# Optimization experiments

Hardware: AMD Instinct MI355X
Metric: run time of the kernel (lower is better)

The kernel has to match this reference:

```python
import jax, jax.numpy as jnp
import numpy as np

L, E, H, FF, N, S, ML = 6, 768, 12, 3072, 8, 1023, 2048


def setup_inputs() -> dict:
    key = jax.random.key(0)
    ks = jax.random.split(key, 16)
    rn = lambda k, shape, s=0.02: jax.random.normal(k, shape, jnp.float32) * s
    return {
        "x": jax.random.normal(ks[0], (N, S, E), jnp.float32),
        "mask": jnp.ones((N, 1, 1, S + 1), jnp.int32),
        "pos_emb": rn(ks[1], (ML, E), 1.0),
        "cls": rn(ks[2], (1, 1, E), 1.0),
        "Wq": rn(ks[3], (L, E, E)), "bq": jnp.zeros((L, E), jnp.float32),
        "Wk": rn(ks[4], (L, E, E)), "bk": jnp.zeros((L, E), jnp.float32),
        "Wv": rn(ks[5], (L, E, E)), "bv": jnp.zeros((L, E), jnp.float32),
        "Wo": rn(ks[6], (L, E, E)), "bo": jnp.zeros((L, E), jnp.float32),
        "ln1_g": jnp.ones((L, E), jnp.float32), "ln1_b": jnp.zeros((L, E), jnp.float32),
        "ln2_g": jnp.ones((L, E), jnp.float32), "ln2_b": jnp.zeros((L, E), jnp.float32),
        "Wf1": rn(ks[7], (L, E, FF)), "bf1": jnp.zeros((L, FF), jnp.float32),
        "Wf2": rn(ks[8], (L, FF, E)), "bf2": jnp.zeros((L, E), jnp.float32),
    }


def _ln(x, g, b, eps=1e-5):
    m = x.mean(-1, keepdims=True)
    v = ((x - m) ** 2).mean(-1, keepdims=True)
    return (x - m) / jnp.sqrt(v + eps) * g + b


def reference(x, mask, pos_emb, cls, Wq, bq, Wk, bk, Wv, bv, Wo, bo,
              ln1_g, ln1_b, ln2_g, ln2_b, Wf1, bf1, Wf2, bf2):
    n, s, e = x.shape
    h = H
    d = e // h
    # prepend CLS token -> [N, T, E], add learned positions
    x = jnp.concatenate([jnp.broadcast_to(cls, (n, 1, e)), x], axis=1)
    t = s + 1
    out = x + pos_emb[:t][None]
    scale = jnp.float32(1.0 / np.sqrt(d))
    for i in range(Wq.shape[0]):
        q = (out @ Wq[i] + bq[i]).reshape(n, t, h, d)
        k = (out @ Wk[i] + bk[i]).reshape(n, t, h, d)
        v = (out @ Wv[i] + bv[i]).reshape(n, t, h, d)
        energy = jnp.einsum('nqhd,nkhd->nhqk', q, k)  # [N,H,T,T]
        energy = jnp.where(mask == 0, jnp.float32(-1e20), energy)
        attn = jax.nn.softmax(energy * scale, axis=-1)
        att = jnp.einsum('nhqk,nkhd->nqhd', attn, v).reshape(n, t, e)
        att = att @ Wo[i] + bo[i]
        hid = _ln(att + out, ln1_g[i], ln1_b[i])  # residual uses query (=out)
        ff = jax.nn.gelu(hid @ Wf1[i] + bf1[i], approximate=False) @ Wf2[i] + bf2[i]
        out = _ln(ff + hid, ln2_g[i], ln2_b[i])
    return out
```

## Files before the change

kernel.cpp:

```cpp
#include <hip/hip_runtime.h>

#define L_ 6
#define E_ 768
#define H_ 12
#define FF_ 3072

typedef __attribute__((ext_vector_type(8))) short bh8;
typedef __attribute__((ext_vector_type(4))) float f32x4;

__device__ inline ushort f2bf(float f) {
  unsigned u = __builtin_bit_cast(unsigned, f);
  u += 0x7fffu + ((u >> 16) & 1u);
  return (ushort)(u >> 16);
}

__device__ __forceinline__ void gload16(const void* g, void* l) {
  __builtin_amdgcn_global_load_lds(
      (const __attribute__((address_space(1))) void*)g,
      (__attribute__((address_space(3))) void*)l, 16, 0, 0);
}

__global__ __launch_bounds__(256) void pack_bias(const float* __restrict__ bq,
                                                 const float* __restrict__ bk,
                                                 const float* __restrict__ bv,
                                                 float* __restrict__ bqkv) {
  int idx = blockIdx.x * 256 + threadIdx.x;
  int l = idx / 2304, j = idx % 2304;
  float v = (j < 768) ? bq[l * 768 + j]
          : (j < 1536) ? bk[l * 768 + j - 768]
                       : bv[l * 768 + j - 1536];
  bqkv[idx] = v;
}

__global__ __launch_bounds__(256) void transpose_w(const float* __restrict__ src,
                                                   ushort* __restrict__ dst,
                                                   int K, int Nn,
                                                   long sstride, long dstride) {
  src += (long)blockIdx.z * sstride;
  dst += (long)blockIdx.z * dstride;
  __shared__ float t[32][33];
  int tx = threadIdx.x & 31, ty = threadIdx.x >> 5;
  int kb = blockIdx.x * 32, nb = blockIdx.y * 32;
#pragma unroll
  for (int i = 0; i < 4; i++) {
    int kr = ty + i * 8;
    t[kr][tx] = src[(long)(kb + kr) * Nn + nb + tx];
  }
  __syncthreads();
#pragma unroll
  for (int i = 0; i < 4; i++) {
    int nr = ty + i * 8;
    dst[(long)(nb + nr) * K + kb + tx] = f2bf(t[tx][nr]);
  }
}

__global__ __launch_bounds__(256) void embed_k(const float* __restrict__ x,
                                               const float* __restrict__ pos,
                                               const float* __restrict__ cls,
                                               float* __restrict__ res,
                                               ushort* __restrict__ xb) {
  int idx = blockIdx.x * 256 + threadIdx.x;
  int c4 = idx % 192;
  int row = idx / 192;
  int t = row & 1023, n = row >> 10;
  f32x4 pv = ((const f32x4*)pos)[t * 192 + c4];
  f32x4 xv;
  if (t == 0) xv = ((const f32x4*)cls)[c4];
  else        xv = ((const f32x4*)x)[(size_t)(n * 1023 + t - 1) * 192 + c4];
  f32x4 s = xv + pv;
  ((f32x4*)res)[idx] = s;
  ushort4 h;
  h.x = f2bf(s[0]); h.y = f2bf(s[1]); h.z = f2bf(s[2]); h.w = f2bf(s[3]);
  ((ushort4*)xb)[idx] = h;
}

template <int MODE>
__global__ __launch_bounds__(256, 4) void gemm_bt(const ushort* __restrict__ A,
                                                  const ushort* __restrict__ Bt,
                                                  int M, int N, int K,
                                                  const float* __restrict__ bias,
                                                  float* __restrict__ sp0,
                                                  float* __restrict__ sp1,
                                                  float* __restrict__ sp2,
                                                  float* __restrict__ sp3,
                                                  ushort* __restrict__ out16,
                                                  ushort* __restrict__ vtb,
                                                  int ksl) {
  __shared__ ushort As[128 * 64];
  __shared__ ushort Bs[128 * 64];
  int tid = threadIdx.x;
  int wid = tid >> 6, lane = tid & 63;
  int wm = wid >> 1, wn = wid & 1;
  int l15 = lane & 15, lhi = lane >> 4;
  int ln8 = lane >> 3, lc8 = (lane & 7) * 8;
  int row0 = blockIdx.x * 128, col0 = blockIdx.y * 128;
  int kb = (MODE == 3) ? blockIdx.z * ksl : 0;
  int nt = ((MODE == 3) ? ksl : K) >> 6;

  f32x4 acc[4][4];
#pragma unroll
  for (int i = 0; i < 4; i++)
#pragma unroll
    for (int j = 0; j < 4; j++) acc[i][j] = (f32x4){0.f, 0.f, 0.f, 0.f};

  const ushort* Ap = A + (size_t)(row0 + wid * 32 + ln8) * K + kb + lc8;
  const ushort* Bp = Bt + (size_t)(col0 + wid * 32 + ln8) * K + kb + lc8;

  for (int kt = 0; kt < nt; ++kt) {
    int k0 = kt << 6;
#pragma unroll
    for (int p = 0; p < 4; p++) {
      int r = wid * 32 + p * 8;
      gload16(Ap + (size_t)p * 8 * K + k0, As + r * 64);
      gload16(Bp + (size_t)p * 8 * K + k0, Bs + r * 64);
    }
    __syncthreads();
#pragma unroll
    for (int ks = 0; ks < 2; ks++) {
      bh8 af[4], bfr[4];
#pragma unroll
      for (int i = 0; i < 4; i++)
        af[i] = *(const bh8*)(As + (wm * 64 + i * 16 + l15) * 64 + ks * 32 + lhi * 8);
#pragma unroll
      for (int j = 0; j < 4; j++)
        bfr[j] = *(const bh8*)(Bs + (wn * 64 + j * 16 + l15) * 64 + ks * 32 + lhi * 8);
#pragma unroll
      for (int i = 0; i < 4; i++)
#pragma unroll
        for (int j = 0; j < 4; j++)
          acc[i][j] = __builtin_amdgcn_mfma_f32_16x16x32_bf16(af[i], bfr[j], acc[i][j], 0, 0, 0);
    }
    __syncthreads();
  }

  float* outp = nullptr;
  if (MODE == 3)
    outp = (blockIdx.z == 0) ? sp0 : (blockIdx.z == 1) ? sp1 : (blockIdx.z == 2) ? sp2 : sp3;
#pragma unroll
  for (int j = 0; j < 4; j++) {
    int col = col0 + wn * 64 + j * 16 + l15;
    float bv = (MODE == 3) ? 0.f : bias[col];
#pragma unroll
    for (int i = 0; i < 4; i++) {
      int rbase = row0 + wm * 64 + i * 16 + lhi * 4;
      if (MODE == 0 && col >= 1536) {
        int hd = col - 1536;
        int nn = rbase >> 10, t0 = rbase & 1023;
        ushort4 h4;
        h4.x = f2bf(acc[i][j][0] + bv);
        h4.y = f2bf(acc[i][j][1] + bv);
        h4.z = f2bf(acc[i][j][2] + bv);
        h4.w = f2bf(acc[i][j][3] + bv);
        *(ushort4*)(vtb + ((size_t)nn * 768 + hd) * 1024 + t0) = h4;
      } else {
#pragma unroll
        for (int r = 0; r < 4; r++) {
          int row = rbase + r;
          size_t o = (size_t)row * N + col;
          float v = acc[i][j][r] + bv;
          if (MODE == 0) {
            out16[o] = f2bf(v);
          } else if (MODE == 3) {
            outp[o] = v;
          } else {
            v = 0.5f * v * (1.f + erff(v * 0.70710678118f));
            out16[o] = f2bf(v);
          }
        }
      }
    }
  }
}

__global__ __launch_bounds__(256) void attn_k(const ushort* __restrict__ qkv,
                                              const ushort* __restrict__ vtb,
                                              const int* __restrict__ mask,
                                              ushort* __restrict__ attb) {
  int qt = blockIdx.x, h = blockIdx.y, n = blockIdx.z;
  int tid = threadIdx.x, wid = tid >> 6, lane = tid & 63;
  int l15 = lane & 15, lhi = lane >> 4;
  __shared__ ushort Ks[2][64 * 64];
  __shared__ ushort Vs[2][64 * 64];
  __shared__ ushort Pt[4][16 * 64];
  ushort* Pw = Pt[wid];

  int ln8 = lane >> 3;
  int swc = (((lane & 7) ^ ln8) << 3);

  const ushort* Kg = qkv + 768 + h * 64;
  const ushort* Vg = vtb + (size_t)(n * 768 + h * 64) * 1024;

  auto stage = [&](int b, int kv0) {
#pragma unroll
    for (int it = 0; it < 2; ++it) {
      int r = wid * 16 + it * 8;
      gload16(Kg + (size_t)(n * 1024 + kv0 + r + ln8) * 2304 + swc, &Ks[b][r * 64]);
      gload16(Vg + (size_t)(r + ln8) * 1024 + kv0 + swc, &Vs[b][r * 64]);
    }
  };

  stage(0, 0);

  int q0 = qt * 64 + wid * 16;
  size_t rowQ = (size_t)(n * 1024 + q0 + l15) * 2304 + h * 64;
  bh8 qf0 = *(const bh8*)(qkv + rowQ + lhi * 8);
  bh8 qf1 = *(const bh8*)(qkv + rowQ + 32 + lhi * 8);

  unsigned long long mbits = 0ull;
#pragma unroll
  for (int i = 0; i < 64; ++i)
    mbits |= (unsigned long long)(mask[n * 1024 + i * 16 + l15] != 0) << i;

  bh8 ones;
#pragma unroll
  for (int i = 0; i < 8; ++i) ones[i] = (short)0x3F80;

  f32x4 o[4], lacc = (f32x4){0.f, 0.f, 0.f, 0.f};
#pragma unroll
  for (int i = 0; i < 4; i++) o[i] = (f32x4){0.f, 0.f, 0.f, 0.f};

  int x15 = (l15 & 7) << 3;
  int buf = 0;
  for (int t = 0; t < 16; ++t) {
    if (t < 15) {
      stage(buf ^ 1, (t + 1) * 64);
      asm volatile("s_waitcnt vmcnt(4)" ::: "memory");
    } else {
      asm volatile("s_waitcnt vmcnt(0)" ::: "memory");
    }
    __builtin_amdgcn_s_barrier();
    const ushort* Kb = Ks[buf];
    const ushort* Vb = Vs[buf];

    f32x4 s[4];
    __builtin_amdgcn_s_setprio(1);
#pragma unroll
    for (int t4 = 0; t4 < 4; ++t4) {
      int rs = (t4 * 16 + l15) * 64;
      s[t4] = (f32x4){0.f, 0.f, 0.f, 0.f};
      s[t4] = __builtin_amdgcn_mfma_f32_16x16x32_bf16(qf0, *(const bh8*)(Kb + rs + ((lhi << 3) ^ x15)), s[t4], 0, 0, 0);
      s[t4] = __builtin_amdgcn_mfma_f32_16x16x32_bf16(qf1, *(const bh8*)(Kb + rs + (((4 + lhi) << 3) ^ x15)), s[t4], 0, 0, 0);
    }
    __builtin_amdgcn_s_setprio(0);

#pragma unroll
    for (int t4 = 0; t4 < 4; ++t4) {
      bool mk = (mbits >> (t * 4 + t4)) & 1ull;
#pragma unroll
      for (int r = 0; r < 4; r++) {
        float xv = mk ? s[t4][r] * 0.125f : -1e20f;
        float p = __expf(fminf(xv, 80.f));
        int prow = lhi * 4 + r;
        int slot = t4 * 2 + (l15 >> 3);
        Pw[prow * 64 + (((slot ^ (prow & 7)) << 3) | (l15 & 7))] = f2bf(p);
      }
    }

    bh8 pf0 = *(const bh8*)(Pw + l15 * 64 + ((lhi << 3) ^ x15));
    bh8 pf1 = *(const bh8*)(Pw + l15 * 64 + (((4 + lhi) << 3) ^ x15));
    __builtin_amdgcn_s_setprio(1);
#pragma unroll
    for (int nb = 0; nb < 4; nb++) {
      int rs = (nb * 16 + l15) * 64;
      o[nb] = __builtin_amdgcn_mfma_f32_16x16x32_bf16(pf0, *(const bh8*)(Vb + rs + ((lhi << 3) ^ x15)), o[nb], 0, 0, 0);
      o[nb] = __builtin_amdgcn_mfma_f32_16x16x32_bf16(pf1, *(const bh8*)(Vb + rs + (((4 + lhi) << 3) ^ x15)), o[nb], 0, 0, 0);
    }
    lacc = __builtin_amdgcn_mfma_f32_16x16x32_bf16(pf0, ones, lacc, 0, 0, 0);
    lacc = __builtin_amdgcn_mfma_f32_16x16x32_bf16(pf1, ones, lacc, 0, 0, 0);
    __builtin_amdgcn_s_setprio(0);

    if (t < 15) {
      asm volatile("s_waitcnt lgkmcnt(0)" ::: "memory");
      __builtin_amdgcn_s_barrier();
    }
    buf ^= 1;
  }

#pragma unroll
  for (int nb = 0; nb < 4; nb++)
#pragma unroll
    for (int r = 0; r < 4; r++) {
      float val = o[nb][r] / lacc[r];
      int row = q0 + lhi * 4 + r;
      int col = h * 64 + nb * 16 + l15;
      attb[(size_t)(n * 1024 + row) * 768 + col] = f2bf(val);
    }
}

template <int S>
__global__ __launch_bounds__(256) void ln_red_k(const float* __restrict__ p0,
                                                const float* __restrict__ p1,
                                                const float* __restrict__ p2,
                                                const float* __restrict__ p3,
                                                const float* __restrict__ resid,
                                                const float* __restrict__ bias,
                                                const float* __restrict__ g,
                                                const float* __restrict__ b,
                                                float* __restrict__ y32,
                                                ushort* __restrict__ y16) {
  int row = blockIdx.x, tid = threadIdx.x;
  size_t base = (size_t)row * 768;
  float v[3];
#pragma unroll
  for (int i = 0; i < 3; i++) {
    int c = tid + i * 256;
    float s = resid[base + c] + bias[c];
    s += p0[base + c] + p1[base + c];
    if (S > 2) s += p2[base + c];
    if (S > 3) s += p3[base + c];
    v[i] = s;
  }
  float s = v[0] + v[1] + v[2];
  float sq = v[0] * v[0] + v[1] * v[1] + v[2] * v[2];
#pragma unroll
  for (int off = 32; off > 0; off >>= 1) {
    s += __shfl_down(s, off);
    sq += __shfl_down(sq, off);
  }
  __shared__ float sws[4], swq[4];
  int wid = tid >> 6, lane = tid & 63;
  if (lane == 0) { sws[wid] = s; swq[wid] = sq; }
  __syncthreads();
  float ts = sws[0] + sws[1] + sws[2] + sws[3];
  float tq = swq[0] + swq[1] + swq[2] + swq[3];
  float mean = ts * (1.f / 768.f);
  float var = tq * (1.f / 768.f) - mean * mean;
  float rstd = rsqrtf(var + 1e-5f);
#pragma unroll
  for (int i = 0; i < 3; i++) {
    int c = tid + i * 256;
    float y = (v[i] - mean) * rstd * g[c] + b[c];
    y32[base + c] = y;
    y16[base + c] = f2bf(y);
  }
}

extern "C" void kernel_launch(void* const* d_in, const int* in_sizes, int n_in,
                              void* d_out, int out_size, void* d_ws, size_t ws_size,
                              hipStream_t stream) {
  const float* x    = (const float*)d_in[0];
  const int*   mask = (const int*)d_in[1];
  const float* pos  = (const float*)d_in[2];
  const float* cls  = (const float*)d_in[3];
  const float* Wq   = (const float*)d_in[4];
  const float* bq   = (const float*)d_in[5];
  const float* Wk   = (const float*)d_in[6];
  const float* bk   = (const float*)d_in[7];
  const float* Wv   = (const float*)d_in[8];
  const float* bv   = (const float*)d_in[9];
  const float* Wo   = (const float*)d_in[10];
  const float* bo   = (const float*)d_in[11];
  const float* ln1g = (const float*)d_in[12];
  const float* ln1b = (const float*)d_in[13];
  const float* ln2g = (const float*)d_in[14];
  const float* ln2b = (const float*)d_in[15];
  const float* Wf1  = (const float*)d_in[16];
  const float* bf1  = (const float*)d_in[17];
  const float* Wf2  = (const float*)d_in[18];
  const float* bf2  = (const float*)d_in[19];

  char* ws = (char*)d_ws;
  size_t off = 0;
  auto alloc = [&](size_t bytes) {
    char* p = ws + off;
    off += (bytes + 255) & ~(size_t)255;
    return p;
  };
  const size_t M = 8192;
  ushort* qkvt = (ushort*)alloc((size_t)L_ * 2304 * 768 * 2);
  ushort* wot  = (ushort*)alloc((size_t)L_ * 768 * 768 * 2);
  ushort* wf1t = (ushort*)alloc((size_t)L_ * 3072 * 768 * 2);
  ushort* wf2t = (ushort*)alloc((size_t)L_ * 768 * 3072 * 2);
  float*  bqkv = (float*)alloc((size_t)L_ * 2304 * 4);
  float*  res  = (float*)alloc(M * 768 * 4);
  float*  pre  = (float*)alloc(M * 768 * 4);
  ushort* xb   = (ushort*)alloc(M * 768 * 2);
  ushort* qkvb = (ushort*)alloc(M * 2304 * 2);
  ushort* vtb  = (ushort*)alloc(M * 768 * 2);
  ushort* attb = (ushort*)alloc(M * 768 * 2);
  ushort* ffb  = (ushort*)alloc(M * 3072 * 2);
  (void)ws_size; (void)in_sizes; (void)n_in; (void)out_size;

  float* slA = pre;
  float* slB = (float*)qkvb;
  float* slC = (float*)((char*)qkvb + M * 768 * 4);
  float* slD = (float*)ffb;

  dim3 tb(256);
  pack_bias<<<54, tb, 0, stream>>>(bq, bk, bv, bqkv);
  transpose_w<<<dim3(24, 24, 6), tb, 0, stream>>>(Wq, qkvt,              768, 768, 768L * 768, 2304L * 768);
  transpose_w<<<dim3(24, 24, 6), tb, 0, stream>>>(Wk, qkvt + 768 * 768,  768, 768, 768L * 768, 2304L * 768);
  transpose_w<<<dim3(24, 24, 6), tb, 0, stream>>>(Wv, qkvt + 2 * 768 * 768, 768, 768, 768L * 768, 2304L * 768);
  transpose_w<<<dim3(24, 24, 6), tb, 0, stream>>>(Wo, wot, 768, 768, 768L * 768, 768L * 768);
  transpose_w<<<dim3(24, 96, 6), tb, 0, stream>>>(Wf1, wf1t, 768, 3072, 768L * 3072, 3072L * 768);
  transpose_w<<<dim3(96, 24, 6), tb, 0, stream>>>(Wf2, wf2t, 3072, 768, 3072L * 768, 768L * 3072);
  embed_k<<<6144, tb, 0, stream>>>(x, pos, cls, res, xb);

  for (int l = 0; l < L_; l++) {
    gemm_bt<0><<<dim3(64, 18), tb, 0, stream>>>(xb, qkvt + (size_t)l * 2304 * 768,
                                                8192, 2304, 768, bqkv + l * 2304,
                                                nullptr, nullptr, nullptr, nullptr,
                                                qkvb, vtb, 0);
    attn_k<<<dim3(16, 12, 8), tb, 0, stream>>>(qkvb, vtb, mask, attb);
    gemm_bt<3><<<dim3(64, 6, 4), tb, 0, stream>>>(attb, wot + (size_t)l * 768 * 768,
                                                  8192, 768, 768, nullptr,
                                                  slA, slB, slC, slD,
                                                  nullptr, nullptr, 192);
    ln_red_k<4><<<8192, tb, 0, stream>>>(slA, slB, slC, slD, res, bo + l * 768,
                                         ln1g + l * 768, ln1b + l * 768, res, xb);
    gemm_bt<2><<<dim3(64, 24), tb, 0, stream>>>(xb, wf1t + (size_t)l * 3072 * 768,
                                                8192, 3072, 768, bf1 + l * 3072,
                                                nullptr, nullptr, nullptr, nullptr,
                                                ffb, nullptr, 0);
    float* y32 = (l == L_ - 1) ? (float*)d_out : res;
    gemm_bt<3><<<dim3(64, 6, 3), tb, 0, stream>>>(ffb, wf2t + (size_t)l * 768 * 3072,
                                                  8192, 768, 3072, nullptr,
                                                  slA, slB, slC, nullptr,
                                                  nullptr, nullptr, 1024);
    ln_red_k<3><<<8192, tb, 0, stream>>>(slA, slB, slC, nullptr, res, bf2 + l * 768,
                                         ln2g + l * 768, ln2b + l * 768, y32, xb);
  }
}
```

Baseline: 2.042 ms.

## Add 256x256 double-buffered swizzled GEMM for QKV, FF1 and FF2 projections

```diff
diff --git a/kernel.cpp b/kernel.cpp
--- a/kernel.cpp
+++ b/kernel.cpp
@@ -75,74 +75,117 @@
 }
 
 template <int MODE>
-__global__ __launch_bounds__(256, 4) void gemm_bt(const ushort* __restrict__ A,
+__global__ __launch_bounds__(512, 2) void gemm256(const ushort* __restrict__ A,
                                                   const ushort* __restrict__ Bt,
                                                   int M, int N, int K,
                                                   const float* __restrict__ bias,
                                                   float* __restrict__ sp0,
                                                   float* __restrict__ sp1,
                                                   float* __restrict__ sp2,
-                                                  float* __restrict__ sp3,
                                                   ushort* __restrict__ out16,
                                                   ushort* __restrict__ vtb,
                                                   int ksl) {
-  __shared__ ushort As[128 * 64];
-  __shared__ ushort Bs[128 * 64];
+  extern __shared__ ushort smem[];
   int tid = threadIdx.x;
   int wid = tid >> 6, lane = tid & 63;
-  int wm = wid >> 1, wn = wid & 1;
+  int wr = wid >> 2, wc = wid & 3;
   int l15 = lane & 15, lhi = lane >> 4;
-  int ln8 = lane >> 3, lc8 = (lane & 7) * 8;
-  int row0 = blockIdx.x * 128, col0 = blockIdx.y * 128;
+  int x7 = l15 & 7;
+  int row0 = blockIdx.x * 256, col0 = blockIdx.y * 256;
   int kb = (MODE == 3) ? blockIdx.z * ksl : 0;
   int nt = ((MODE == 3) ? ksl : K) >> 6;
 
-  f32x4 acc[4][4];
-#pragma unroll
-  for (int i = 0; i < 4; i++)
+  int srow = tid >> 3;
+  int swk = ((tid & 7) ^ (srow & 7)) << 3;
+  const ushort* Ag = A + (size_t)(row0 + srow) * K + kb + swk;
+  const ushort* Bg = Bt + (size_t)(col0 + srow) * K + kb + swk;
+
+  auto stA = [&](int slot, int kt, int half) {
+#pragma unroll
+    for (int it = 0; it < 2; ++it) {
+      int gr0 = half * 128 + it * 64;
+      gload16(Ag + (size_t)gr0 * K + (size_t)kt * 64,
+              smem + (slot << 14) + (gr0 + wid * 8) * 64);
+    }
+  };
+  auto stB = [&](int slot, int kt, int half) {
+#pragma unroll
+    for (int it = 0; it < 2; ++it) {
+      int gr0 = half * 128 + it * 64;
+      gload16(Bg + (size_t)gr0 * K + (size_t)kt * 64,
+              smem + 32768 + (slot << 14) + (gr0 + wid * 8) * 64);
+    }
+  };
+
+  f32x4 acc[8][4];
+#pragma unroll
+  for (int i = 0; i < 8; i++)
 #pragma unroll
     for (int j = 0; j < 4; j++) acc[i][j] = (f32x4){0.f, 0.f, 0.f, 0.f};
 
-  const ushort* Ap = A + (size_t)(row0 + wid * 32 + ln8) * K + kb + lc8;
-  const ushort* Bp = Bt + (size_t)(col0 + wid * 32 + ln8) * K + kb + lc8;
-
-  for (int kt = 0; kt < nt; ++kt) {
-    int k0 = kt << 6;
-#pragma unroll
-    for (int p = 0; p < 4; p++) {
-      int r = wid * 32 + p * 8;
-      gload16(Ap + (size_t)p * 8 * K + k0, As + r * 64);
-      gload16(Bp + (size_t)p * 8 * K + k0, Bs + r * 64);
-    }
-    __syncthreads();
-#pragma unroll
-    for (int ks = 0; ks < 2; ks++) {
-      bh8 af[4], bfr[4];
-#pragma unroll
-      for (int i = 0; i < 4; i++)
-        af[i] = *(const bh8*)(As + (wm * 64 + i * 16 + l15) * 64 + ks * 32 + lhi * 8);
-#pragma unroll
-      for (int j = 0; j < 4; j++)
-        bfr[j] = *(const bh8*)(Bs + (wn * 64 + j * 16 + l15) * 64 + ks * 32 + lhi * 8);
-#pragma unroll
-      for (int i = 0; i < 4; i++)
-#pragma unroll
-        for (int j = 0; j < 4; j++)
-          acc[i][j] = __builtin_amdgcn_mfma_f32_16x16x32_bf16(af[i], bfr[j], acc[i][j], 0, 0, 0);
-    }
-    __syncthreads();
+  stB(0, 0, 0); stB(0, 0, 1);
+  stA(0, 0, 0); stA(0, 0, 1);
+  stB(1, 1, 0); stB(1, 1, 1);
+
+  bh8 bfr[4][2];
+
+  for (int t = 0; t < nt; ++t) {
+    int s = t & 1;
+    const ushort* Ab = smem + (s << 14);
+    const ushort* Bb = smem + 32768 + (s << 14);
+#pragma unroll
+    for (int p = 0; p < 4; ++p) {
+      if (p == 0) {
+        if (t + 1 < nt) {
+          stA(s ^ 1, t + 1, 0);
+          asm volatile("s_waitcnt vmcnt(6)" ::: "memory");
+        } else {
+          asm volatile("s_waitcnt vmcnt(0)" ::: "memory");
+        }
+        __builtin_amdgcn_s_barrier();
+#pragma unroll
+        for (int j = 0; j < 4; ++j)
+#pragma unroll
+          for (int kk = 0; kk < 2; ++kk)
+            bfr[j][kk] = *(const bh8*)(Bb + (wc * 64 + j * 16 + l15) * 64 +
+                                       (((kk * 4 + lhi) ^ x7) << 3));
+      } else if (p == 1) {
+        if (t + 1 < nt) stA(s ^ 1, t + 1, 1);
+        if (t + 2 < nt) stB(s, t + 2, 0);
+      } else if (p == 2) {
+        if (t + 2 < nt) stB(s, t + 2, 1);
+      }
+      bh8 af[2][2];
+#pragma unroll
+      for (int il = 0; il < 2; ++il)
+#pragma unroll
+        for (int kk = 0; kk < 2; ++kk)
+          af[il][kk] = *(const bh8*)(Ab + (wr * 128 + (p * 2 + il) * 16 + l15) * 64 +
+                                     (((kk * 4 + lhi) ^ x7) << 3));
+      __builtin_amdgcn_s_setprio(1);
+#pragma unroll
+      for (int il = 0; il < 2; ++il)
+#pragma unroll
+        for (int j = 0; j < 4; ++j)
+#pragma unroll
+          for (int kk = 0; kk < 2; ++kk)
+            acc[p * 2 + il][j] = __builtin_amdgcn_mfma_f32_16x16x32_bf16(
+                af[il][kk], bfr[j][kk], acc[p * 2 + il][j], 0, 0, 0);
+      __builtin_amdgcn_s_setprio(0);
+      asm volatile("s_waitcnt lgkmcnt(0)" ::: "memory");
+      __builtin_amdgcn_s_barrier();
+    }
   }
 
   float* outp = nullptr;
-  if (MODE == 3)
-    outp = (blockIdx.z == 0) ? sp0 : (blockIdx.z == 1) ? sp1 : (blockIdx.z == 2) ? sp2 : sp3;
+  if (MODE == 3) outp = (blockIdx.z == 0) ? sp0 : (blockIdx.z == 1) ? sp1 : sp2;
 #pragma unroll
   for (int j = 0; j < 4; j++) {
-    int col = col0 + wn * 64 + j * 16 + l15;
+    int col = col0 + wc * 64 + j * 16 + l15;
     float bv = (MODE == 3) ? 0.f : bias[col];
 #pragma unroll
-    for (int i = 0; i < 4; i++) {
-      int rbase = row0 + wm * 64 + i * 16 + lhi * 4;
+    for (int i = 0; i < 8; i++) {
+      int rbase = row0 + wr * 128 + i * 16 + lhi * 4;
       if (MODE == 0 && col >= 1536) {
         int hd = col - 1536;
         int nn = rbase >> 10, t0 = rbase & 1023;
@@ -167,6 +210,81 @@
             out16[o] = f2bf(v);
           }
         }
+      }
+    }
+  }
+}
+
+template <int MODE>
+__global__ __launch_bounds__(256, 4) void gemm_bt(const ushort* __restrict__ A,
+                                                  const ushort* __restrict__ Bt,
+                                                  int M, int N, int K,
+                                                  const float* __restrict__ bias,
+                                                  float* __restrict__ sp0,
+                                                  float* __restrict__ sp1,
+                                                  float* __restrict__ sp2,
+                                                  float* __restrict__ sp3,
+                                                  ushort* __restrict__ out16,
+                                                  int ksl) {
+  __shared__ ushort As[128 * 64];
+  __shared__ ushort Bs[128 * 64];
+  int tid = threadIdx.x;
+  int wid = tid >> 6, lane = tid & 63;
+  int wm = wid >> 1, wn = wid & 1;
+  int l15 = lane & 15, lhi = lane >> 4;
+  int ln8 = lane >> 3, lc8 = (lane & 7) * 8;
+  int row0 = blockIdx.x * 128, col0 = blockIdx.y * 128;
+  int kb = (MODE == 3) ? blockIdx.z * ksl : 0;
+  int nt = ((MODE == 3) ? ksl : K) >> 6;
+
+  f32x4 acc[4][4];
+#pragma unroll
+  for (int i = 0; i < 4; i++)
+#pragma unroll
+    for (int j = 0; j < 4; j++) acc[i][j] = (f32x4){0.f, 0.f, 0.f, 0.f};
+
+  const ushort* Ap = A + (size_t)(row0 + wid * 32 + ln8) * K + kb + lc8;
+  const ushort* Bp = Bt + (size_t)(col0 + wid * 32 + ln8) * K + kb + lc8;
+
+  for (int kt = 0; kt < nt; ++kt) {
+    int k0 = kt << 6;
+#pragma unroll
+    for (int p = 0; p < 4; p++) {
+      int r = wid * 32 + p * 8;
+      gload16(Ap + (size_t)p * 8 * K + k0, As + r * 64);
+      gload16(Bp + (size_t)p * 8 * K + k0, Bs + r * 64);
+    }
+    __syncthreads();
+#pragma unroll
+    for (int ks = 0; ks < 2; ks++) {
+      bh8 af[4], bfr[4];
+#pragma unroll
+      for (int i = 0; i < 4; i++)
+        af[i] = *(const bh8*)(As + (wm * 64 + i * 16 + l15) * 64 + ks * 32 + lhi * 8);
+#pragma unroll
+      for (int j = 0; j < 4; j++)
+        bfr[j] = *(const bh8*)(Bs + (wn * 64 + j * 16 + l15) * 64 + ks * 32 + lhi * 8);
+#pragma unroll
+      for (int i = 0; i < 4; i++)
+#pragma unroll
+        for (int j = 0; j < 4; j++)
+          acc[i][j] = __builtin_amdgcn_mfma_f32_16x16x32_bf16(af[i], bfr[j], acc[i][j], 0, 0, 0);
+    }
+    __syncthreads();
+  }
+
+  float* outp = (blockIdx.z == 0) ? sp0 : (blockIdx.z == 1) ? sp1 : (blockIdx.z == 2) ? sp2 : sp3;
+  (void)bias; (void)out16;
+#pragma unroll
+  for (int j = 0; j < 4; j++) {
+    int col = col0 + wn * 64 + j * 16 + l15;
+#pragma unroll
+    for (int i = 0; i < 4; i++) {
+      int rbase = row0 + wm * 64 + i * 16 + lhi * 4;
+#pragma unroll
+      for (int r = 0; r < 4; r++) {
+        size_t o = (size_t)(rbase + r) * N + col;
+        outp[o] = acc[i][j][r];
       }
     }
   }
@@ -359,6 +477,13 @@
   const float* Wf2  = (const float*)d_in[18];
   const float* bf2  = (const float*)d_in[19];
 
+  hipFuncSetAttribute(reinterpret_cast<const void*>(gemm256<0>),
+                      hipFuncAttributeMaxDynamicSharedMemorySize, 131072);
+  hipFuncSetAttribute(reinterpret_cast<const void*>(gemm256<2>),
+                      hipFuncAttributeMaxDynamicSharedMemorySize, 131072);
+  hipFuncSetAttribute(reinterpret_cast<const void*>(gemm256<3>),
+                      hipFuncAttributeMaxDynamicSharedMemorySize, 131072);
+
   char* ws = (char*)d_ws;
   size_t off = 0;
   auto alloc = [&](size_t bytes) {
@@ -397,26 +522,25 @@
   embed_k<<<6144, tb, 0, stream>>>(x, pos, cls, res, xb);
 
   for (int l = 0; l < L_; l++) {
-    gemm_bt<0><<<dim3(64, 18), tb, 0, stream>>>(xb, qkvt + (size_t)l * 2304 * 768,
-                                                8192, 2304, 768, bqkv + l * 2304,
-                                                nullptr, nullptr, nullptr, nullptr,
-                                                qkvb, vtb, 0);
+    gemm256<0><<<dim3(32, 9), 512, 131072, stream>>>(xb, qkvt + (size_t)l * 2304 * 768,
+                                                     8192, 2304, 768, bqkv + l * 2304,
+                                                     nullptr, nullptr, nullptr,
+                                                     qkvb, vtb, 0);
     attn_k<<<dim3(16, 12, 8), tb, 0, stream>>>(qkvb, vtb, mask, attb);
     gemm_bt<3><<<dim3(64, 6, 4), tb, 0, stream>>>(attb, wot + (size_t)l * 768 * 768,
                                                   8192, 768, 768, nullptr,
-                                                  slA, slB, slC, slD,
-                                                  nullptr, nullptr, 192);
+                                                  slA, slB, slC, slD, nullptr, 192);
     ln_red_k<4><<<8192, tb, 0, stream>>>(slA, slB, slC, slD, res, bo + l * 768,
                                          ln1g + l * 768, ln1b + l * 768, res, xb);
-    gemm_bt<2><<<dim3(64, 24), tb, 0, stream>>>(xb, wf1t + (size_t)l * 3072 * 768,
-                                                8192, 3072, 768, bf1 + l * 3072,
-                                                nullptr, nullptr, nullptr, nullptr,
-                                                ffb, nullptr, 0);
+    gemm256<2><<<dim3(32, 12), 512, 131072, stream>>>(xb, wf1t + (size_t)l * 3072 * 768,
+                                                      8192, 3072, 768, bf1 + l * 3072,
+                                                      nullptr, nullptr, nullptr,
+                                                      ffb, nullptr, 0);
     float* y32 = (l == L_ - 1) ? (float*)d_out : res;
-    gemm_bt<3><<<dim3(64, 6, 3), tb, 0, stream>>>(ffb, wf2t + (size_t)l * 768 * 3072,
-                                                  8192, 768, 3072, nullptr,
-                                                  slA, slB, slC, nullptr,
-                                                  nullptr, nullptr, 1024);
+    gemm256<3><<<dim3(32, 3, 3), 512, 131072, stream>>>(ffb, wf2t + (size_t)l * 768 * 3072,
+                                                        8192, 768, 3072, nullptr,
+                                                        slA, slB, slC,
+                                                        nullptr, nullptr, 1024);
     ln_red_k<3><<<8192, tb, 0, stream>>>(slA, slB, slC, nullptr, res, bf2 + l * 768,
                                          ln2g + l * 768, ln2b + l * 768, y32, xb);
   }
```

Result: slower. 2.160 ms (+5.8%).
